# Performance work log

Hardware: AMD Instinct MI355X
Metric: run time of the kernel (lower is better)

Reference implementation:

```python
import jax, jax.numpy as jnp
import numpy as np
import math

D = 128      # d_model == num_filters
L = 4        # num_conv_layers
K = 7        # kernel_size
H = 8        # num_heads
B, S = 64, 400


def setup_inputs() -> dict:
    key = jax.random.key(0)
    ks = jax.random.split(key, 24)
    s = 0.02
    inp = {}
    inp['x'] = jax.random.normal(ks[0], (B, S, D), dtype=jnp.float32)
    # per-conv-layer params (stacked over L)
    inp['ln_g'] = jnp.ones((L, D), jnp.float32)
    inp['ln_b'] = jnp.zeros((L, D), jnp.float32)
    inp['dw_w'] = jax.random.normal(ks[1], (L, D, D, K), dtype=jnp.float32) * s
    inp['dw_b'] = jnp.zeros((L, D), jnp.float32)
    inp['pw_w'] = jax.random.normal(ks[2], (L, D, D), dtype=jnp.float32) * s
    inp['pw_b'] = jnp.zeros((L, D), jnp.float32)
    # attention block
    inp['attln_g'] = jnp.ones((D,), jnp.float32)
    inp['attln_b'] = jnp.zeros((D,), jnp.float32)
    inp['wq'] = jax.random.normal(ks[3], (D, D), dtype=jnp.float32) * s
    inp['bq'] = jnp.zeros((D,), jnp.float32)
    inp['wk'] = jax.random.normal(ks[4], (D, D), dtype=jnp.float32) * s
    inp['bk'] = jnp.zeros((D,), jnp.float32)
    inp['wv'] = jax.random.normal(ks[5], (D, D), dtype=jnp.float32) * s
    inp['bv'] = jnp.zeros((D,), jnp.float32)
    inp['wp'] = jax.random.normal(ks[6], (D, D), dtype=jnp.float32) * s
    inp['bp'] = jnp.zeros((D,), jnp.float32)
    # ffn
    inp['ffnln_g'] = jnp.ones((D,), jnp.float32)
    inp['ffnln_b'] = jnp.zeros((D,), jnp.float32)
    inp['fc_w'] = jax.random.normal(ks[7], (D, D), dtype=jnp.float32) * s
    inp['fc_b'] = jnp.zeros((D,), jnp.float32)
    return inp


def _layernorm(x, g, b, eps=1e-5):
    mu = jnp.mean(x, axis=-1, keepdims=True)
    var = jnp.var(x, axis=-1, keepdims=True)
    return (x - mu) * jax.lax.rsqrt(var + eps) * g + b


def _pos_encoding(seq_len, channels, dtype):
    pos = jnp.arange(seq_len, dtype=dtype)                       # [S]
    freq = 1.0 / (10000.0 ** (jnp.arange(0, channels, 2, dtype=dtype) / channels))
    sin_inp = pos[:, None] * freq[None, :]                       # [S, C/2]
    return jnp.concatenate([jnp.sin(sin_inp), jnp.cos(sin_inp)], axis=-1)  # [S, C]


def _encoder_fwd(x, ln_g, ln_b, dw_w, dw_b, pw_w, pw_b,
                 attln_g, attln_b, wq, bq, wk, bk, wv, bv, wp, bp,
                 ffnln_g, ffnln_b, fc_w, fc_b):
    b, s, d = x.shape
    out = x + _pos_encoding(s, d, x.dtype)[None, :, :]

    # conv stack: LN -> transpose -> (full) conv K -> pointwise conv -> transpose
    pad = dw_w.shape[-1] // 2
    for i in range(dw_w.shape[0]):
        h = _layernorm(out, ln_g[i], ln_b[i])
        t = jnp.transpose(h, (0, 2, 1))                          # [B, D, S]
        t = jax.lax.conv_general_dilated(
            t, dw_w[i], window_strides=(1,), padding=[(pad, pad)],
            dimension_numbers=('NCH', 'OIH', 'NCH')) + dw_b[i][None, :, None]
        t = jnp.einsum('bds,fd->bfs', t, pw_w[i]) + pw_b[i][None, :, None]
        out = jnp.transpose(t, (0, 2, 1))                        # [B, S, D]

    # causal self-attention (explicit scores, per original)
    h = _layernorm(out, attln_g, attln_b)
    hd = d // H
    q = (jnp.einsum('bsd,od->bso', h, wq) + bq).reshape(b, s, H, hd)
    k = (jnp.einsum('bsd,od->bso', h, wk) + bk).reshape(b, s, H, hd)
    v = (jnp.einsum('bsd,od->bso', h, wv) + bv).reshape(b, s, H, hd)
    att = jnp.einsum('bqhd,bkhd->bhqk', q, k) / math.sqrt(hd)    # [B, H, S, S]
    causal = jnp.tril(jnp.ones((s, s), dtype=bool))
    att = jnp.where(causal[None, None], att, jnp.asarray(-1e10, att.dtype))
    att = jax.nn.softmax(att, axis=-1)
    y = jnp.einsum('bhqk,bkhd->bqhd', att, v).reshape(b, s, d)
    y = jnp.einsum('bsd,od->bso', y, wp) + bp

    # ffn
    y = _layernorm(y, ffnln_g, ffnln_b)
    y = jnp.einsum('bsd,od->bso', y, fc_w) + fc_b
    return jax.nn.relu(y)


def reference(x, ln_g, ln_b, dw_w, dw_b, pw_w, pw_b,
              attln_g, attln_b, wq, bq, wk, bk, wv, bv, wp, bp,
              ffnln_g, ffnln_b, fc_w, fc_b):
    return _encoder_fwd(x, ln_g, ln_b, dw_w, dw_b, pw_w, pw_b,
                        attln_g, attln_b, wq, bq, wk, bk, wv, bv, wp, bp,
                        ffnln_g, ffnln_b, fc_w, fc_b)
```

## Files before the change

kernel.cpp:

```cpp
#include <hip/hip_runtime.h>
#include <hip/hip_bf16.h>
#include <math.h>

#define Dm 128
#define Lc 4
#define Kc 7
#define Hh 8
#define Bb 64
#define Ss 400
#define SsP 448
#define TOK (Bb*Ss)

typedef __attribute__((ext_vector_type(8))) short bf16x8;
typedef __attribute__((ext_vector_type(4))) float f32x4;

__device__ __forceinline__ float bf2f(unsigned int u) {
    union { unsigned int i; float f; } x; x.i = u << 16; return x.f;
}
__device__ __forceinline__ unsigned short f2bf(float f) {
    __hip_bfloat16 h = __float2bfloat16(f);
    return __builtin_bit_cast(unsigned short, h);
}
__device__ __forceinline__ unsigned int packbf(float a, float b) {
    return (unsigned int)f2bf(a) | ((unsigned int)f2bf(b) << 16);
}


__global__ __launch_bounds__(256) void prep_all(const float* __restrict__ wq, const float* __restrict__ wk,
                                                const float* __restrict__ wv, const float* __restrict__ wp,
                                                const float* __restrict__ fc,
                                                const float* __restrict__ pw_w, const float* __restrict__ dw_w,
                                                const float* __restrict__ dw_b, const float* __restrict__ pw_b,
                                                float* __restrict__ pe, unsigned short* __restrict__ wf,
                                                float* __restrict__ mb, unsigned short* __restrict__ mwf) {
    __shared__ unsigned short hiS[64][136];
    __shared__ unsigned short loS[64][136];
    int blk = blockIdx.x;
    int tid = threadIdx.x;
    if (blk < 200) {
        int s = blk * 2 + (tid >> 7);
        int c = tid & 127;
        int j = (c < 64) ? c : (c - 64);
        float freq = expf(-(2.0f * j / 128.0f) * 9.210340371976184f);
        float a = (float)s * freq;
        pe[s * Dm + c] = (c < 64) ? sinf(a) : cosf(a);
        return;
    }
    if (blk < 520) {
        int idx = (blk - 200) * 256 + tid;
        int m = idx >> 14;
        int r = idx & 16383;
        int fragi = r >> 9, lr = (r >> 3) & 63, j = r & 7;
        int kb = fragi >> 3, nb = fragi & 7;
        int o = nb * 16 + (lr & 15);
        int d = kb * 32 + (lr >> 4) * 8 + j;
        const float* src = (m == 0) ? wq : (m == 1) ? wk : (m == 2) ? wv : (m == 3) ? wp : fc;
        wf[idx] = f2bf(src[o * Dm + d]);
        return;
    }
    if (blk < 524) {
        int l = blk - 520;
        int f = tid;
        if (f < Dm) {
            const float* pwl = pw_w + ((size_t)l * Dm + f) * Dm;
            const float* db  = dw_b + l * Dm;
            float acc = pw_b[l * Dm + f];
            #pragma unroll 8
            for (int c4 = 0; c4 < 32; ++c4) {
                float4 p = *(const float4*)(pwl + c4 * 4);
                float4 d = *(const float4*)(db + c4 * 4);
                acc += p.x * d.x + p.y * d.y + p.z * d.z + p.w * d.w;
            }
            mb[l * Dm + f] = acc;
        }
        return;
    }
    int mblk = blk - 524;
    int ih = mblk & 1;
    int k  = (mblk >> 1) % 7;
    int l  = mblk / 14;
    int lane = tid & 63, w = tid >> 6;

    const float* dwl = dw_w + (size_t)l * (Dm * Dm * Kc) + k;
    for (int it = 0; it < 32; ++it) {
        int idx = it * 256 + tid;
        int c = idx >> 6, il = idx & 63;
        int i = ih * 64 + il;
        float x = dwl[(size_t)(c * Dm + i) * Kc];
        unsigned short hi = f2bf(x);
        float lo = x - bf2f(hi);
        hiS[il][c] = hi;
        loS[il][c] = f2bf(lo);
    }
    __syncthreads();

    const float* pwl = pw_w + (size_t)l * Dm * Dm;
    int arow = lane & 15, ac = (lane >> 4) * 8;
    f32x4 acc[2][4];
    #pragma unroll
    for (int n = 0; n < 2; ++n)
        #pragma unroll
        for (int m = 0; m < 4; ++m) acc[n][m] = (f32x4){0.f, 0.f, 0.f, 0.f};

    #pragma unroll
    for (int kb = 0; kb < 4; ++kb) {
        int c0 = kb * 32 + ac;
        bf16x8 Bhi[2], Blo[2];
        #pragma unroll
        for (int n = 0; n < 2; ++n) {
            int f = (w * 2 + n) * 16 + arow;
            const float* rp = pwl + (size_t)f * Dm + c0;
            float4 a = *(const float4*)rp;
            float4 b = *(const float4*)(rp + 4);
            float v[8] = {a.x, a.y, a.z, a.w, b.x, b.y, b.z, b.w};
            unsigned short hh[8], ll[8];
            #pragma unroll
            for (int j = 0; j < 8; ++j) {
                hh[j] = f2bf(v[j]);
                ll[j] = f2bf(v[j] - bf2f(hh[j]));
            }
            uint4 uh = make_uint4((unsigned)hh[0] | ((unsigned)hh[1] << 16),
                                  (unsigned)hh[2] | ((unsigned)hh[3] << 16),
                                  (unsigned)hh[4] | ((unsigned)hh[5] << 16),
                                  (unsigned)hh[6] | ((unsigned)hh[7] << 16));
            uint4 ul = make_uint4((unsigned)ll[0] | ((unsigned)ll[1] << 16),
                                  (unsigned)ll[2] | ((unsigned)ll[3] << 16),
                                  (unsigned)ll[4] | ((unsigned)ll[5] << 16),
                                  (unsigned)ll[6] | ((unsigned)ll[7] << 16));
            Bhi[n] = __builtin_bit_cast(bf16x8, uh);
            Blo[n] = __builtin_bit_cast(bf16x8, ul);
        }
        #pragma unroll
        for (int m = 0; m < 4; ++m) {
            bf16x8 ahi = *(const bf16x8*)&hiS[m * 16 + arow][c0];
            bf16x8 alo = *(const bf16x8*)&loS[m * 16 + arow][c0];
            #pragma unroll
            for (int n = 0; n < 2; ++n) {
                acc[n][m] = __builtin_amdgcn_mfma_f32_16x16x32_bf16(ahi, Bhi[n], acc[n][m], 0, 0, 0);
                acc[n][m] = __builtin_amdgcn_mfma_f32_16x16x32_bf16(ahi, Blo[n], acc[n][m], 0, 0, 0);
                acc[n][m] = __builtin_amdgcn_mfma_f32_16x16x32_bf16(alo, Bhi[n], acc[n][m], 0, 0, 0);
            }
        }
    }
    #pragma unroll
    for (int n = 0; n < 2; ++n) {
        int nb = w * 2 + n;
        #pragma unroll
        for (int m = 0; m < 4; ++m) {
            int i0 = ih * 64 + m * 16 + (lane >> 4) * 4;
            int ib = i0 >> 5, i32 = i0 & 31;
            int lanep = ((i32 >> 3) << 4) | arow;
            int jb = i32 & 7;
            size_t frag = ((size_t)(l * 28 + (k * 4 + ib)) * 8 + nb);
            *(uint2*)(mwf + frag * 512 + lanep * 8 + jb) =
                make_uint2(packbf(acc[n][m][0], acc[n][m][1]),
                           packbf(acc[n][m][2], acc[n][m][3]));
        }
    }
}


__device__ __forceinline__ uint4 ln_pack(float4 v0, float4 v1,
                                         const float* __restrict__ g,
                                         const float* __restrict__ b, int c16) {
    float sum = v0.x + v0.y + v0.z + v0.w + v1.x + v1.y + v1.z + v1.w;
    float sq  = v0.x*v0.x + v0.y*v0.y + v0.z*v0.z + v0.w*v0.w
              + v1.x*v1.x + v1.y*v1.y + v1.z*v1.z + v1.w*v1.w;
    #pragma unroll
    for (int off = 8; off; off >>= 1) {
        sum += __shfl_xor(sum, off);
        sq  += __shfl_xor(sq, off);
    }
    float mu = sum * (1.0f / 128.0f);
    float var = sq * (1.0f / 128.0f) - mu * mu;
    float rs = rsqrtf(var + 1e-5f);
    float4 g0 = *(const float4*)(g + c16 * 8);
    float4 g1 = *(const float4*)(g + c16 * 8 + 4);
    float4 b0 = *(const float4*)(b + c16 * 8);
    float4 b1 = *(const float4*)(b + c16 * 8 + 4);
    uint4 o;
    o.x = packbf((v0.x - mu) * rs * g0.x + b0.x, (v0.y - mu) * rs * g0.y + b0.y);
    o.y = packbf((v0.z - mu) * rs * g0.z + b0.z, (v0.w - mu) * rs * g0.w + b0.w);
    o.z = packbf((v1.x - mu) * rs * g1.x + b1.x, (v1.y - mu) * rs * g1.y + b1.y);
    o.w = packbf((v1.z - mu) * rs * g1.z + b1.z, (v1.w - mu) * rs * g1.w + b1.w);
    return o;
}


__global__ __launch_bounds__(256) void conv_mfma(const float* __restrict__ in,
                                                 const float* __restrict__ pe,
                                                 const unsigned short* __restrict__ mwf,
                                                 const float* __restrict__ mb,
                                                 const float* __restrict__ lng,
                                                 const float* __restrict__ lnb,
                                                 float* __restrict__ out) {
    __shared__ unsigned short hs[54][136];
    int tid = threadIdx.x;
    int lane = tid & 63, w = tid >> 6;
    int bI = blockIdx.x / 9;
    int st = blockIdx.x % 9;
    int s0 = st * 48;
    const float* ib = in + (size_t)bI * Ss * Dm;
    for (int c = tid; c < 54 * 16; c += 256) {
        int row = c >> 4, c16 = c & 15;
        int gs = s0 - 3 + row;
        if (gs >= 0 && gs < Ss) {
            const float* rp = ib + (size_t)gs * Dm + c16 * 8;
            float4 v0 = *(const float4*)rp;
            float4 v1 = *(const float4*)(rp + 4);
            if (pe) {
                const float* pp = pe + (size_t)gs * Dm + c16 * 8;
                float4 p0 = *(const float4*)pp;
                float4 p1 = *(const float4*)(pp + 4);
                v0.x += p0.x; v0.y += p0.y; v0.z += p0.z; v0.w += p0.w;
                v1.x += p1.x; v1.y += p1.y; v1.z += p1.z; v1.w += p1.w;
            }
            *(uint4*)&hs[row][c16 * 8] = ln_pack(v0, v1, lng, lnb, c16);
        } else {
            *(uint4*)&hs[row][c16 * 8] = make_uint4(0u, 0u, 0u, 0u);
        }
    }
    __syncthreads();

    f32x4 acc[2][3];
    #pragma unroll
    for (int n = 0; n < 2; ++n)
        #pragma unroll
        for (int m = 0; m < 3; ++m) acc[n][m] = (f32x4){0.f, 0.f, 0.f, 0.f};

    int nb0 = w * 2;
    int arow = lane & 15, acol = (lane >> 4) * 8;
    #pragma unroll 4
    for (int kb = 0; kb < 28; ++kb) {
        int k = kb >> 2, i0 = (kb & 3) * 32;
        bf16x8 b0 = *(const bf16x8*)(mwf + ((size_t)(kb * 8 + nb0)) * 512 + lane * 8);
        bf16x8 b1 = *(const bf16x8*)(mwf + ((size_t)(kb * 8 + nb0 + 1)) * 512 + lane * 8);
        #pragma unroll
        for (int m = 0; m < 3; ++m) {
            bf16x8 af = *(const bf16x8*)&hs[m * 16 + arow + k][i0 + acol];
            acc[0][m] = __builtin_amdgcn_mfma_f32_16x16x32_bf16(af, b0, acc[0][m], 0, 0, 0);
            acc[1][m] = __builtin_amdgcn_mfma_f32_16x16x32_bf16(af, b1, acc[1][m], 0, 0, 0);
        }
    }
    int rr = (lane >> 4) * 4;
    #pragma unroll
    for (int n = 0; n < 2; ++n) {
        int f0 = (nb0 + n) * 16;
        float bias = mb[f0 + arow];
        #pragma unroll
        for (int m = 0; m < 3; ++m)
            #pragma unroll
            for (int r = 0; r < 4; ++r) {
                int s = s0 + m * 16 + rr + r;
                if (s < Ss)
                    out[((size_t)bI * Ss + s) * Dm + f0 + arow] = acc[n][m][r] + bias;
            }
    }
}


__global__ __launch_bounds__(256) void qkv_mfma(const float* __restrict__ in,
                                                const float* __restrict__ lng,
                                                const float* __restrict__ lnb,
                                                const unsigned short* __restrict__ wfb,
                                                const float* __restrict__ bq,
                                                const float* __restrict__ bk,
                                                const float* __restrict__ bv,
                                                unsigned short* __restrict__ Qo,
                                                unsigned short* __restrict__ Ko,
                                                unsigned short* __restrict__ Vo) {
    __shared__ unsigned short hs[80][136];
    int tid = threadIdx.x;
    int lane = tid & 63, w = tid >> 6;
    int y = blockIdx.y;
    int bI = blockIdx.x / 5;
    int sb = (blockIdx.x % 5) * 80;
    const float* ib = in + ((size_t)bI * Ss + sb) * Dm;
    for (int c = tid; c < 80 * 16; c += 256) {
        int row = c >> 4, c16 = c & 15;
        const float* rp = ib + (size_t)row * Dm + c16 * 8;
        float4 v0 = *(const float4*)rp;
        float4 v1 = *(const float4*)(rp + 4);
        *(uint4*)&hs[row][c16 * 8] = ln_pack(v0, v1, lng, lnb, c16);
    }
    __syncthreads();

    int nb0 = w * 2;
    int arow = lane & 15, acol = (lane >> 4) * 8;
    int nmat = (y == 0) ? 2 : 1;
    for (int mi = 0; mi < nmat; ++mi) {
        int mat = (y == 0) ? mi : 2;
        const unsigned short* wf = wfb + (size_t)mat * 16384;
        f32x4 acc[2][5];
        #pragma unroll
        for (int n = 0; n < 2; ++n)
            #pragma unroll
            for (int m = 0; m < 5; ++m) acc[n][m] = (f32x4){0.f, 0.f, 0.f, 0.f};
        #pragma unroll
        for (int kb = 0; kb < 4; ++kb) {
            bf16x8 b0 = *(const bf16x8*)(wf + ((size_t)(kb * 8 + nb0)) * 512 + lane * 8);
            bf16x8 b1 = *(const bf16x8*)(wf + ((size_t)(kb * 8 + nb0 + 1)) * 512 + lane * 8);
            #pragma unroll
            for (int m = 0; m < 5; ++m) {
                bf16x8 af = *(const bf16x8*)&hs[m * 16 + arow][kb * 32 + acol];
                acc[0][m] = __builtin_amdgcn_mfma_f32_16x16x32_bf16(af, b0, acc[0][m], 0, 0, 0);
                acc[1][m] = __builtin_amdgcn_mfma_f32_16x16x32_bf16(af, b1, acc[1][m], 0, 0, 0);
            }
        }
        int rr = (lane >> 4) * 4;
        const float* bias = (mat == 0) ? bq : (mat == 1) ? bk : bv;
        float sc = (mat == 0) ? 0.25f : 1.0f;
        #pragma unroll
        for (int n = 0; n < 2; ++n) {
            int hI = nb0 + n;
            float bvv = bias[hI * 16 + arow];
            if (mat < 2) {
                unsigned short* qo = (mat == 0) ? Qo : Ko;
                #pragma unroll
                for (int m = 0; m < 5; ++m)
                    #pragma unroll
                    for (int r = 0; r < 4; ++r) {
                        int s = sb + m * 16 + rr + r;
                        qo[(((size_t)(bI * Hh + hI)) * Ss + s) * 16 + arow] = f2bf((acc[n][m][r] + bvv) * sc);
                    }
            } else {
                unsigned short* base = Vo + ((size_t)(bI * Hh + hI) * 16 + arow) * SsP + sb;
                #pragma unroll
                for (int m = 0; m < 5; ++m) {
                    unsigned lo = packbf(acc[n][m][0] + bvv, acc[n][m][1] + bvv);
                    unsigned hi = packbf(acc[n][m][2] + bvv, acc[n][m][3] + bvv);
                    *(uint2*)(base + m * 16 + rr) = make_uint2(lo, hi);
                }
            }
        }
    }
}


__global__ __launch_bounds__(256) void gemm2(const void* __restrict__ inv,
                                             const unsigned short* __restrict__ wf,
                                             const float* __restrict__ bias,
                                             const float* __restrict__ lng,
                                             const float* __restrict__ lnb,
                                             float* __restrict__ out, int relu) {
    __shared__ unsigned short hs[80][136];
    int tid = threadIdx.x;
    int lane = tid & 63, w = tid >> 6;
    size_t tok0 = (size_t)blockIdx.x * 80;
    if (lng) {
        const float* ib = (const float*)inv + tok0 * Dm;
        for (int c = tid; c < 80 * 16; c += 256) {
            int row = c >> 4, c16 = c & 15;
            const float* rp = ib + (size_t)row * Dm + c16 * 8;
            float4 v0 = *(const float4*)rp;
            float4 v1 = *(const float4*)(rp + 4);
            *(uint4*)&hs[row][c16 * 8] = ln_pack(v0, v1, lng, lnb, c16);
        }
    } else {
        const unsigned short* ib = (const unsigned short*)inv + tok0 * Dm;
        for (int c = tid; c < 80 * 16; c += 256) {
            int row = c >> 4, c16 = c & 15;
            *(uint4*)&hs[row][c16 * 8] = *(const uint4*)(ib + (size_t)row * Dm + c16 * 8);
        }
    }
    __syncthreads();

    f32x4 acc[2][5];
    #pragma unroll
    for (int n = 0; n < 2; ++n)
        #pragma unroll
        for (int m = 0; m < 5; ++m) acc[n][m] = (f32x4){0.f, 0.f, 0.f, 0.f};

    int nb0 = w * 2;
    int arow = lane & 15, acol = (lane >> 4) * 8;
    #pragma unroll
    for (int kb = 0; kb < 4; ++kb) {
        bf16x8 b0 = *(const bf16x8*)(wf + ((size_t)(kb * 8 + nb0)) * 512 + lane * 8);
        bf16x8 b1 = *(const bf16x8*)(wf + ((size_t)(kb * 8 + nb0 + 1)) * 512 + lane * 8);
        #pragma unroll
        for (int m = 0; m < 5; ++m) {
            bf16x8 af = *(const bf16x8*)&hs[m * 16 + arow][kb * 32 + acol];
            acc[0][m] = __builtin_amdgcn_mfma_f32_16x16x32_bf16(af, b0, acc[0][m], 0, 0, 0);
            acc[1][m] = __builtin_amdgcn_mfma_f32_16x16x32_bf16(af, b1, acc[1][m], 0, 0, 0);
        }
    }
    int rr = (lane >> 4) * 4;
    #pragma unroll
    for (int n = 0; n < 2; ++n) {
        int f0 = (nb0 + n) * 16;
        float bvv = bias[f0 + arow];
        #pragma unroll
        for (int m = 0; m < 5; ++m)
            #pragma unroll
            for (int r = 0; r < 4; ++r) {
                float v = acc[n][m][r] + bvv;
                if (relu) v = fmaxf(v, 0.f);
                out[(tok0 + m * 16 + rr + r) * Dm + f0 + arow] = v;
            }
    }
}


__global__ __launch_bounds__(256) void attn_mfma(const unsigned short* __restrict__ Q,
                                                 const unsigned short* __restrict__ Kb,
                                                 const unsigned short* __restrict__ VT,
                                                 unsigned short* __restrict__ out) {
    int wid = threadIdx.x >> 6, lane = threadIdx.x & 63;
    int gw = blockIdx.x * 4 + wid;
    int bh = gw & 511, qt = gw >> 9;
    int q15 = lane & 15, h = lane >> 4;
    int qg = qt * 16 + q15;

    uint4 qv = make_uint4(0u, 0u, 0u, 0u);
    if (h < 2) qv = *(const uint4*)(Q + ((size_t)bh * Ss + qg) * 16 + h * 8);
    bf16x8 qf = __builtin_bit_cast(bf16x8, qv);

    f32x4 o = (f32x4){0.f, 0.f, 0.f, 0.f};
    float mrow = -1e30f, lrow = 0.f;
    const unsigned short* kbase = Kb + (size_t)bh * Ss * 16;
    const unsigned short* vbase = VT + ((size_t)bh * 16 + q15) * SsP;
    int srcA = q15 + ((h & 1) << 5);
    int srcB = srcA + 16;
    bool t1 = h >= 2;
    f32x4 z = (f32x4){0.f, 0.f, 0.f, 0.f};

    for (int kt0 = 0; kt0 <= qt; kt0 += 4) {
        uint4 kv[4];
        #pragma unroll
        for (int t = 0; t < 4; ++t) {
            kv[t] = make_uint4(0u, 0u, 0u, 0u);
            if (h < 2 && kt0 + t <= qt)
                kv[t] = *(const uint4*)(kbase + (size_t)((kt0 + t) * 16 + q15) * 16 + h * 8);
        }
        f32x4 s[4];
        #pragma unroll
        for (int t = 0; t < 4; ++t)
            s[t] = __builtin_amdgcn_mfma_f32_16x16x32_bf16(__builtin_bit_cast(bf16x8, kv[t]), qf, z, 0, 0, 0);

        float p[16];
        #pragma unroll
        for (int t = 0; t < 4; ++t)
            #pragma unroll
            for (int r = 0; r < 4; ++r) {
                int ka = (kt0 + t) * 16 + h * 4 + r;
                p[t * 4 + r] = (ka <= qg) ? s[t][r] : -1e30f;
            }
        float tm = p[0];
        #pragma unroll
        for (int i = 1; i < 16; ++i) tm = fmaxf(tm, p[i]);
        tm = fmaxf(tm, __shfl_xor(tm, 16));
        tm = fmaxf(tm, __shfl_xor(tm, 32));
        float mnew = fmaxf(mrow, tm);
        float corr = __expf(mrow - mnew);
        float psum = 0.f;
        #pragma unroll
        for (int i = 0; i < 16; ++i) { p[i] = __expf(p[i] - mnew); psum += p[i]; }
        psum += __shfl_xor(psum, 16);
        psum += __shfl_xor(psum, 32);
        lrow = lrow * corr + psum;
        mrow = mnew;
        o[0] *= corr; o[1] *= corr; o[2] *= corr; o[3] *= corr;

        #pragma unroll
        for (int pr = 0; pr < 2; ++pr) {
            const float* pp = p + pr * 8;
            unsigned pk0 = packbf(pp[0], pp[1]), pk1 = packbf(pp[2], pp[3]);
            unsigned pk2 = packbf(pp[4], pp[5]), pk3 = packbf(pp[6], pp[7]);
            unsigned a0 = __shfl(pk0, srcA), a1 = __shfl(pk1, srcA);
            unsigned a2 = __shfl(pk0, srcB), a3 = __shfl(pk1, srcB);
            unsigned b0 = __shfl(pk2, srcA), b1 = __shfl(pk3, srcA);
            unsigned b2 = __shfl(pk2, srcB), b3 = __shfl(pk3, srcB);
            uint4 pw = make_uint4(t1 ? b0 : a0, t1 ? b1 : a1, t1 ? b2 : a2, t1 ? b3 : a3);
            uint4 vv = *(const uint4*)(vbase + (kt0 + pr * 2) * 16 + h * 8);
            o = __builtin_amdgcn_mfma_f32_16x16x32_bf16(__builtin_bit_cast(bf16x8, vv),
                                                        __builtin_bit_cast(bf16x8, pw), o, 0, 0, 0);
        }
    }
    float inv = 1.0f / lrow;
    int bI = bh >> 3, hh = bh & 7;
    unsigned short* op = out + ((size_t)bI * Ss + qg) * Dm + hh * 16 + h * 4;
    *(uint2*)op = make_uint2(packbf(o[0] * inv, o[1] * inv),
                             packbf(o[2] * inv, o[3] * inv));
}


extern "C" void kernel_launch(void* const* d_in, const int* in_sizes, int n_in,
                              void* d_out, int out_size, void* d_ws, size_t ws_size,
                              hipStream_t stream) {
    (void)in_sizes; (void)n_in; (void)out_size; (void)ws_size;
    const float* x       = (const float*)d_in[0];
    const float* ln_g    = (const float*)d_in[1];
    const float* ln_b    = (const float*)d_in[2];
    const float* dw_w    = (const float*)d_in[3];
    const float* dw_b    = (const float*)d_in[4];
    const float* pw_w    = (const float*)d_in[5];
    const float* pw_b    = (const float*)d_in[6];
    const float* attln_g = (const float*)d_in[7];
    const float* attln_b = (const float*)d_in[8];
    const float* wq = (const float*)d_in[9];
    const float* bq = (const float*)d_in[10];
    const float* wk = (const float*)d_in[11];
    const float* bk = (const float*)d_in[12];
    const float* wv = (const float*)d_in[13];
    const float* bv = (const float*)d_in[14];
    const float* wp = (const float*)d_in[15];
    const float* bp = (const float*)d_in[16];
    const float* ffnln_g = (const float*)d_in[17];
    const float* ffnln_b = (const float*)d_in[18];
    const float* fc_w = (const float*)d_in[19];
    const float* fc_b = (const float*)d_in[20];

    float* ws = (float*)d_ws;
    float* pe = ws;
    float* mb = pe + 51200;
    float* C1 = mb + 512;
    float* C2 = C1 + 3276800;
    unsigned short* mwf = (unsigned short*)(C2 + 3276800);
    unsigned short* wfb = mwf + 458752;
    unsigned short* Qb  = wfb + 81920;
    unsigned short* Kb2 = Qb + 3276800;
    unsigned short* VTb = Kb2 + 3276800;
    unsigned short* A1b = VTb + 3670016;

    prep_all<<<580, 256, 0, stream>>>(wq, wk, wv, wp, fc_w, pw_w, dw_w, dw_b, pw_b,
                                      pe, wfb, mb, mwf);

    conv_mfma<<<Bb * 9, 256, 0, stream>>>(x,  pe,      mwf,                    mb,           ln_g,           ln_b,           C1);
    conv_mfma<<<Bb * 9, 256, 0, stream>>>(C1, nullptr, mwf + 114688,           mb + Dm,      ln_g + Dm,      ln_b + Dm,      C2);
    conv_mfma<<<Bb * 9, 256, 0, stream>>>(C2, nullptr, mwf + 2 * 114688,       mb + 2 * Dm,  ln_g + 2 * Dm,  ln_b + 2 * Dm,  C1);
    conv_mfma<<<Bb * 9, 256, 0, stream>>>(C1, nullptr, mwf + 3 * 114688,       mb + 3 * Dm,  ln_g + 3 * Dm,  ln_b + 3 * Dm,  C2);

    qkv_mfma<<<dim3(320, 2), 256, 0, stream>>>(C2, attln_g, attln_b, wfb, bq, bk, bv, Qb, Kb2, VTb);
    attn_mfma<<<3200, 256, 0, stream>>>(Qb, Kb2, VTb, A1b);
    gemm2<<<320, 256, 0, stream>>>(A1b, wfb + 3 * 16384, bp, nullptr, nullptr, C1, 0);

    gemm2<<<320, 256, 0, stream>>>(C1, wfb + 4 * 16384, fc_b, ffnln_g, ffnln_b, (float*)d_out, 1);
}
```

Baseline: 128.4 us.

## Store intermediate activations in bf16 and reshape conv/attention thread mappings

Conv layer outputs and the attention projection output are now written and read as bf16 instead of fp32, which halves the global memory traffic between the chained kernels. The conv kernel moves to 512 threads with one 16-column output slice per wave, doubling wave-level parallelism. Attention is relaunched on a 2D grid with 5 waves per block, so each block covers one batch-head and five query tiles. The bf16 round-trip between layers adds some rounding error to the activations.

After: 122.7 us. 4.5% less time.

```diff
diff --git a/kernel.cpp b/kernel.cpp
--- a/kernel.cpp
+++ b/kernel.cpp
@@ -160,12 +160,12 @@
 }
 
 
-__device__ __forceinline__ uint4 ln_pack(float4 v0, float4 v1,
+__device__ __forceinline__ uint4 ln_core(float v[8],
                                          const float* __restrict__ g,
                                          const float* __restrict__ b, int c16) {
-    float sum = v0.x + v0.y + v0.z + v0.w + v1.x + v1.y + v1.z + v1.w;
-    float sq  = v0.x*v0.x + v0.y*v0.y + v0.z*v0.z + v0.w*v0.w
-              + v1.x*v1.x + v1.y*v1.y + v1.z*v1.z + v1.w*v1.w;
+    float sum = 0.f, sq = 0.f;
+    #pragma unroll
+    for (int j = 0; j < 8; ++j) { sum += v[j]; sq += v[j] * v[j]; }
     #pragma unroll
     for (int off = 8; off; off >>= 1) {
         sum += __shfl_xor(sum, off);
@@ -179,87 +179,88 @@
     float4 b0 = *(const float4*)(b + c16 * 8);
     float4 b1 = *(const float4*)(b + c16 * 8 + 4);
     uint4 o;
-    o.x = packbf((v0.x - mu) * rs * g0.x + b0.x, (v0.y - mu) * rs * g0.y + b0.y);
-    o.y = packbf((v0.z - mu) * rs * g0.z + b0.z, (v0.w - mu) * rs * g0.w + b0.w);
-    o.z = packbf((v1.x - mu) * rs * g1.x + b1.x, (v1.y - mu) * rs * g1.y + b1.y);
-    o.w = packbf((v1.z - mu) * rs * g1.z + b1.z, (v1.w - mu) * rs * g1.w + b1.w);
+    o.x = packbf((v[0] - mu) * rs * g0.x + b0.x, (v[1] - mu) * rs * g0.y + b0.y);
+    o.y = packbf((v[2] - mu) * rs * g0.z + b0.z, (v[3] - mu) * rs * g0.w + b0.w);
+    o.z = packbf((v[4] - mu) * rs * g1.x + b1.x, (v[5] - mu) * rs * g1.y + b1.y);
+    o.w = packbf((v[6] - mu) * rs * g1.z + b1.z, (v[7] - mu) * rs * g1.w + b1.w);
     return o;
 }
 
-
-__global__ __launch_bounds__(256) void conv_mfma(const float* __restrict__ in,
+__device__ __forceinline__ uint4 ln_pack_bf(const unsigned short* __restrict__ rp,
+                                            const float* __restrict__ g,
+                                            const float* __restrict__ b, int c16) {
+    uint4 u = *(const uint4*)rp;
+    float v[8] = { bf2f(u.x & 0xffffu), bf2f(u.x >> 16), bf2f(u.y & 0xffffu), bf2f(u.y >> 16),
+                   bf2f(u.z & 0xffffu), bf2f(u.z >> 16), bf2f(u.w & 0xffffu), bf2f(u.w >> 16) };
+    return ln_core(v, g, b, c16);
+}
+
+
+__global__ __launch_bounds__(512) void conv_mfma(const unsigned short* __restrict__ in16,
+                                                 const float* __restrict__ in32,
                                                  const float* __restrict__ pe,
                                                  const unsigned short* __restrict__ mwf,
                                                  const float* __restrict__ mb,
                                                  const float* __restrict__ lng,
                                                  const float* __restrict__ lnb,
-                                                 float* __restrict__ out) {
+                                                 unsigned short* __restrict__ out) {
     __shared__ unsigned short hs[54][136];
     int tid = threadIdx.x;
     int lane = tid & 63, w = tid >> 6;
     int bI = blockIdx.x / 9;
     int st = blockIdx.x % 9;
     int s0 = st * 48;
-    const float* ib = in + (size_t)bI * Ss * Dm;
-    for (int c = tid; c < 54 * 16; c += 256) {
+    for (int c = tid; c < 54 * 16; c += 512) {
         int row = c >> 4, c16 = c & 15;
         int gs = s0 - 3 + row;
+        uint4 o = make_uint4(0u, 0u, 0u, 0u);
         if (gs >= 0 && gs < Ss) {
-            const float* rp = ib + (size_t)gs * Dm + c16 * 8;
-            float4 v0 = *(const float4*)rp;
-            float4 v1 = *(const float4*)(rp + 4);
-            if (pe) {
+            if (in32) {
+                const float* rp = in32 + ((size_t)bI * Ss + gs) * Dm + c16 * 8;
                 const float* pp = pe + (size_t)gs * Dm + c16 * 8;
-                float4 p0 = *(const float4*)pp;
-                float4 p1 = *(const float4*)(pp + 4);
-                v0.x += p0.x; v0.y += p0.y; v0.z += p0.z; v0.w += p0.w;
-                v1.x += p1.x; v1.y += p1.y; v1.z += p1.z; v1.w += p1.w;
-            }
-            *(uint4*)&hs[row][c16 * 8] = ln_pack(v0, v1, lng, lnb, c16);
-        } else {
-            *(uint4*)&hs[row][c16 * 8] = make_uint4(0u, 0u, 0u, 0u);
-        }
+                float v[8];
+                #pragma unroll
+                for (int j = 0; j < 8; ++j) v[j] = rp[j] + pp[j];
+                o = ln_core(v, lng, lnb, c16);
+            } else {
+                o = ln_pack_bf(in16 + ((size_t)bI * Ss + gs) * Dm + c16 * 8, lng, lnb, c16);
+            }
+        }
+        *(uint4*)&hs[row][c16 * 8] = o;
     }
     __syncthreads();
 
-    f32x4 acc[2][3];
-    #pragma unroll
-    for (int n = 0; n < 2; ++n)
-        #pragma unroll
-        for (int m = 0; m < 3; ++m) acc[n][m] = (f32x4){0.f, 0.f, 0.f, 0.f};
-
-    int nb0 = w * 2;
+    f32x4 acc[3];
+    #pragma unroll
+    for (int m = 0; m < 3; ++m) acc[m] = (f32x4){0.f, 0.f, 0.f, 0.f};
+
+    int nb = w;
     int arow = lane & 15, acol = (lane >> 4) * 8;
     #pragma unroll 4
     for (int kb = 0; kb < 28; ++kb) {
         int k = kb >> 2, i0 = (kb & 3) * 32;
-        bf16x8 b0 = *(const bf16x8*)(mwf + ((size_t)(kb * 8 + nb0)) * 512 + lane * 8);
-        bf16x8 b1 = *(const bf16x8*)(mwf + ((size_t)(kb * 8 + nb0 + 1)) * 512 + lane * 8);
+        bf16x8 bfr = *(const bf16x8*)(mwf + ((size_t)(kb * 8 + nb)) * 512 + lane * 8);
         #pragma unroll
         for (int m = 0; m < 3; ++m) {
             bf16x8 af = *(const bf16x8*)&hs[m * 16 + arow + k][i0 + acol];
-            acc[0][m] = __builtin_amdgcn_mfma_f32_16x16x32_bf16(af, b0, acc[0][m], 0, 0, 0);
-            acc[1][m] = __builtin_amdgcn_mfma_f32_16x16x32_bf16(af, b1, acc[1][m], 0, 0, 0);
+            acc[m] = __builtin_amdgcn_mfma_f32_16x16x32_bf16(af, bfr, acc[m], 0, 0, 0);
         }
     }
     int rr = (lane >> 4) * 4;
-    #pragma unroll
-    for (int n = 0; n < 2; ++n) {
-        int f0 = (nb0 + n) * 16;
-        float bias = mb[f0 + arow];
-        #pragma unroll
-        for (int m = 0; m < 3; ++m)
-            #pragma unroll
-            for (int r = 0; r < 4; ++r) {
-                int s = s0 + m * 16 + rr + r;
-                if (s < Ss)
-                    out[((size_t)bI * Ss + s) * Dm + f0 + arow] = acc[n][m][r] + bias;
-            }
-    }
-}
-
-
-__global__ __launch_bounds__(256) void qkv_mfma(const float* __restrict__ in,
+    int f0 = nb * 16;
+    float bias = mb[f0 + arow];
+    #pragma unroll
+    for (int m = 0; m < 3; ++m)
+        #pragma unroll
+        for (int r = 0; r < 4; ++r) {
+            int s = s0 + m * 16 + rr + r;
+            if (s < Ss)
+                out[((size_t)bI * Ss + s) * Dm + f0 + arow] = f2bf(acc[m][r] + bias);
+        }
+}
+
+
+__global__ __launch_bounds__(256) void qkv_mfma(const unsigned short* __restrict__ in,
                                                 const float* __restrict__ lng,
                                                 const float* __restrict__ lnb,
                                                 const unsigned short* __restrict__ wfb,
@@ -275,13 +276,10 @@
     int y = blockIdx.y;
     int bI = blockIdx.x / 5;
     int sb = (blockIdx.x % 5) * 80;
-    const float* ib = in + ((size_t)bI * Ss + sb) * Dm;
+    const unsigned short* ib = in + ((size_t)bI * Ss + sb) * Dm;
     for (int c = tid; c < 80 * 16; c += 256) {
         int row = c >> 4, c16 = c & 15;
-        const float* rp = ib + (size_t)row * Dm + c16 * 8;
-        float4 v0 = *(const float4*)rp;
-        float4 v1 = *(const float4*)(rp + 4);
-        *(uint4*)&hs[row][c16 * 8] = ln_pack(v0, v1, lng, lnb, c16);
+        *(uint4*)&hs[row][c16 * 8] = ln_pack_bf(ib + (size_t)row * Dm + c16 * 8, lng, lnb, c16);
     }
     __syncthreads();
 
@@ -337,27 +335,23 @@
 }
 
 
-__global__ __launch_bounds__(256) void gemm2(const void* __restrict__ inv,
+__global__ __launch_bounds__(256) void gemm2(const unsigned short* __restrict__ in,
                                              const unsigned short* __restrict__ wf,
                                              const float* __restrict__ bias,
                                              const float* __restrict__ lng,
                                              const float* __restrict__ lnb,
-                                             float* __restrict__ out, int relu) {
+                                             void* __restrict__ outv, int mode) {
     __shared__ unsigned short hs[80][136];
     int tid = threadIdx.x;
     int lane = tid & 63, w = tid >> 6;
     size_t tok0 = (size_t)blockIdx.x * 80;
+    const unsigned short* ib = in + tok0 * Dm;
     if (lng) {
-        const float* ib = (const float*)inv + tok0 * Dm;
         for (int c = tid; c < 80 * 16; c += 256) {
             int row = c >> 4, c16 = c & 15;
-            const float* rp = ib + (size_t)row * Dm + c16 * 8;
-            float4 v0 = *(const float4*)rp;
-            float4 v1 = *(const float4*)(rp + 4);
-            *(uint4*)&hs[row][c16 * 8] = ln_pack(v0, v1, lng, lnb, c16);
+            *(uint4*)&hs[row][c16 * 8] = ln_pack_bf(ib + (size_t)row * Dm + c16 * 8, lng, lnb, c16);
         }
     } else {
-        const unsigned short* ib = (const unsigned short*)inv + tok0 * Dm;
         for (int c = tid; c < 80 * 16; c += 256) {
             int row = c >> 4, c16 = c & 15;
             *(uint4*)&hs[row][c16 * 8] = *(const uint4*)(ib + (size_t)row * Dm + c16 * 8);
@@ -394,20 +388,23 @@
             #pragma unroll
             for (int r = 0; r < 4; ++r) {
                 float v = acc[n][m][r] + bvv;
-                if (relu) v = fmaxf(v, 0.f);
-                out[(tok0 + m * 16 + rr + r) * Dm + f0 + arow] = v;
-            }
-    }
-}
-
-
-__global__ __launch_bounds__(256) void attn_mfma(const unsigned short* __restrict__ Q,
+                if (mode == 1) {
+                    ((float*)outv)[(tok0 + m * 16 + rr + r) * Dm + f0 + arow] = fmaxf(v, 0.f);
+                } else {
+                    ((unsigned short*)outv)[(tok0 + m * 16 + rr + r) * Dm + f0 + arow] = f2bf(v);
+                }
+            }
+    }
+}
+
+
+__global__ __launch_bounds__(320) void attn_mfma(const unsigned short* __restrict__ Q,
                                                  const unsigned short* __restrict__ Kb,
                                                  const unsigned short* __restrict__ VT,
                                                  unsigned short* __restrict__ out) {
     int wid = threadIdx.x >> 6, lane = threadIdx.x & 63;
-    int gw = blockIdx.x * 4 + wid;
-    int bh = gw & 511, qt = gw >> 9;
+    int bh = blockIdx.x;
+    int qt = blockIdx.y * 5 + wid;
     int q15 = lane & 15, h = lane >> 4;
     int qg = qt * 16 + q15;
 
@@ -513,11 +510,11 @@
     float* ws = (float*)d_ws;
     float* pe = ws;
     float* mb = pe + 51200;
-    float* C1 = mb + 512;
-    float* C2 = C1 + 3276800;
-    unsigned short* mwf = (unsigned short*)(C2 + 3276800);
+    unsigned short* mwf = (unsigned short*)(mb + 512);
     unsigned short* wfb = mwf + 458752;
-    unsigned short* Qb  = wfb + 81920;
+    unsigned short* C1  = wfb + 81920;
+    unsigned short* C2  = C1 + 3276800;
+    unsigned short* Qb  = C2 + 3276800;
     unsigned short* Kb2 = Qb + 3276800;
     unsigned short* VTb = Kb2 + 3276800;
     unsigned short* A1b = VTb + 3670016;
@@ -525,14 +522,14 @@
     prep_all<<<580, 256, 0, stream>>>(wq, wk, wv, wp, fc_w, pw_w, dw_w, dw_b, pw_b,
                                       pe, wfb, mb, mwf);
 
-    conv_mfma<<<Bb * 9, 256, 0, stream>>>(x,  pe,      mwf,                    mb,           ln_g,           ln_b,           C1);
-    conv_mfma<<<Bb * 9, 256, 0, stream>>>(C1, nullptr, mwf + 114688,           mb + Dm,      ln_g + Dm,      ln_b + Dm,      C2);
-    conv_mfma<<<Bb * 9, 256, 0, stream>>>(C2, nullptr, mwf + 2 * 114688,       mb + 2 * Dm,  ln_g + 2 * Dm,  ln_b + 2 * Dm,  C1);
-    conv_mfma<<<Bb * 9, 256, 0, stream>>>(C1, nullptr, mwf + 3 * 114688,       mb + 3 * Dm,  ln_g + 3 * Dm,  ln_b + 3 * Dm,  C2);
+    conv_mfma<<<Bb * 9, 512, 0, stream>>>(nullptr, x, pe, mwf,              mb,          ln_g,          ln_b,          C1);
+    conv_mfma<<<Bb * 9, 512, 0, stream>>>(C1, nullptr, nullptr, mwf + 114688,     mb + Dm,     ln_g + Dm,     ln_b + Dm,     C2);
+    conv_mfma<<<Bb * 9, 512, 0, stream>>>(C2, nullptr, nullptr, mwf + 2 * 114688, mb + 2 * Dm, ln_g + 2 * Dm, ln_b + 2 * Dm, C1);
+    conv_mfma<<<Bb * 9, 512, 0, stream>>>(C1, nullptr, nullptr, mwf + 3 * 114688, mb + 3 * Dm, ln_g + 3 * Dm, ln_b + 3 * Dm, C2);
 
     qkv_mfma<<<dim3(320, 2), 256, 0, stream>>>(C2, attln_g, attln_b, wfb, bq, bk, bv, Qb, Kb2, VTb);
-    attn_mfma<<<3200, 256, 0, stream>>>(Qb, Kb2, VTb, A1b);
+    attn_mfma<<<dim3(512, 5), 320, 0, stream>>>(Qb, Kb2, VTb, A1b);
     gemm2<<<320, 256, 0, stream>>>(A1b, wfb + 3 * 16384, bp, nullptr, nullptr, C1, 0);
 
-    gemm2<<<320, 256, 0, stream>>>(C1, wfb + 4 * 16384, fc_b, ffnln_g, ffnln_b, (float*)d_out, 1);
-}
+    gemm2<<<320, 256, 0, stream>>>(C1, wfb + 4 * 16384, fc_b, ffnln_g, ffnln_b, d_out, 1);
+}
```
